# Kernel optimization log

Hardware: AMD Instinct MI355X
Metric: run time of the kernel (lower is better)

## Reference

```python
import jax, jax.numpy as jnp
import numpy as np

NUM_SKILLS = 1000
DIM_S = 64
SIZE_M = 64
B, T = 64, 200


def setup_inputs() -> dict:
    key = jax.random.key(0)
    ks = jax.random.split(key, 16)
    skills = jax.random.randint(ks[0], (B, T), 0, NUM_SKILLS)
    responses = jax.random.randint(ks[1], (B, T), 0, 2)
    s = 1.0 / np.sqrt(DIM_S)
    return {
        "skills": skills,
        "responses": responses,
        "k_emb": jax.random.normal(ks[2], (NUM_SKILLS, DIM_S)) * s,
        "v_emb": jax.random.normal(ks[3], (2 * NUM_SKILLS, DIM_S)) * s,
        "Mk": jax.random.normal(ks[4], (SIZE_M, DIM_S)) * np.sqrt(2.0 / DIM_S),
        "Mv0": jax.random.normal(ks[5], (SIZE_M, DIM_S)) * np.sqrt(2.0 / DIM_S),
        "fW": jax.random.normal(ks[6], (DIM_S, 2 * DIM_S)) * (1.0 / np.sqrt(2 * DIM_S)),
        "fb": jnp.zeros((DIM_S,)),
        "eW": jax.random.normal(ks[7], (DIM_S, DIM_S)) * s,
        "eb": jnp.zeros((DIM_S,)),
        "aW": jax.random.normal(ks[8], (DIM_S, DIM_S)) * s,
        "ab": jnp.zeros((DIM_S,)),
        "pW": jax.random.normal(ks[9], (1, DIM_S)) * s,
        "pb": jnp.zeros((1,)),
    }


def reference(skills, responses, k_emb, v_emb, Mk, Mv0, fW, fb, eW, eb, aW, ab, pW, pb):
    # dropout is identity in eval mode
    masked_r = responses * (responses > -1).astype(responses.dtype)
    x = skills + NUM_SKILLS * masked_r            # [B, T]
    k = k_emb[skills]                              # [B, T, D]
    v = v_emb[x]                                   # [B, T, D]
    w = jax.nn.softmax(jnp.einsum('btd,md->btm', k, Mk), axis=-1)  # [B, T, M]
    e = jax.nn.sigmoid(v @ eW.T + eb)              # [B, T, D]
    a = jnp.tanh(v @ aW.T + ab)                    # [B, T, D]

    Mv_init = jnp.broadcast_to(Mv0, (skills.shape[0],) + Mv0.shape)  # [B, M, D]

    def step(Mvt, inp):
        wt, et, at = inp                           # [B,M], [B,D], [B,D]
        read = jnp.einsum('bm,bmd->bd', wt, Mvt)   # read BEFORE update (Mv[:, :-1])
        Mvt = Mvt * (1.0 - wt[:, :, None] * et[:, None, :]) + wt[:, :, None] * at[:, None, :]
        return Mvt, read

    xs = (jnp.swapaxes(w, 0, 1), jnp.swapaxes(e, 0, 1), jnp.swapaxes(a, 0, 1))
    _, reads = jax.lax.scan(step, Mv_init, xs)     # reads: [T, B, D]
    reads = jnp.swapaxes(reads, 0, 1)              # [B, T, D]

    f = jnp.tanh(jnp.concatenate([reads, k], axis=-1) @ fW.T + fb)  # [B, T, D]
    p = jax.nn.sigmoid(f @ pW.T + pb)[..., 0]      # [B, T]
    return p[:, 1:]                                # pred, [B, T-1]
```

## Files before the change

kernel.cpp:

```cpp
#include <hip/hip_runtime.h>
#include <stdint.h>

#define NSK 1000
#define TT  200
#define BB  64
#define NROW (BB * TT)
#define NOUT (BB * (TT-1))
#define CH  20
#define RW  4

__device__ __forceinline__ unsigned ulane_bcast(unsigned v, int l) {
  return __builtin_amdgcn_readlane(v, l);
}
__device__ __forceinline__ float frcp(float x) { return __builtin_amdgcn_rcpf(x); }
__device__ __forceinline__ float sigm(float x) { return frcp(1.f + __expf(-x)); }
__device__ __forceinline__ float tanh_fast(float x) {
  return fmaf(-2.f, frcp(1.f + __expf(2.f * x)), 1.f);
}

typedef _Float16 half2v __attribute__((ext_vector_type(2)));
typedef _Float16 v8h __attribute__((ext_vector_type(8)));
typedef float    v4f __attribute__((ext_vector_type(4)));
union H2U { unsigned u; half2v h; };
__device__ __forceinline__ unsigned pack2h(float a, float b) {
  H2U x; x.h = (half2v){(_Float16)a, (_Float16)b}; return x.u;
}
__device__ __forceinline__ unsigned short f16bits(float x) {
  H2U u; u.h = (half2v){(_Float16)x, (_Float16)0.f}; return (unsigned short)(u.u & 0xffffu);
}
__device__ __forceinline__ float f16lo(unsigned bits) {
  H2U u; u.u = bits; return (float)u.h.x;
}
__device__ __forceinline__ float f16hi(unsigned bits) {
  H2U u; u.u = bits; return (float)u.h.y;
}
__device__ __forceinline__ float dot2h(unsigned sp, unsigned wp, float acc) {
#if __has_builtin(__builtin_amdgcn_fdot2)
  H2U s, w; s.u = sp; w.u = wp;
  return __builtin_amdgcn_fdot2(s.h, w.h, acc, false);
#else
  H2U s, w; s.u = sp; w.u = wp;
  return fmaf((float)s.h.y, (float)w.h.y, fmaf((float)s.h.x, (float)w.h.x, acc));
#endif
}
__device__ __forceinline__ unsigned pack_pairs(float v) {
  const int lane = threadIdx.x & 63;
  float a = __shfl(v, 2 * lane);
  float b = __shfl(v, 2 * lane + 1);
  return pack2h(a, b);
}
__device__ __forceinline__ v8h pk8(float4 x0, float4 x1) {
  return (v8h){(_Float16)x0.x, (_Float16)x0.y, (_Float16)x0.z, (_Float16)x0.w,
               (_Float16)x1.x, (_Float16)x1.y, (_Float16)x1.z, (_Float16)x1.w};
}

__global__ __launch_bounds__(128) void wea_mfma(
    const int* __restrict__ skills, const int* __restrict__ responses,
    const float* __restrict__ k_emb, const float* __restrict__ v_emb,
    const float* __restrict__ Mk, const float* __restrict__ eW,
    const float* __restrict__ eb, const float* __restrict__ aW,
    const float* __restrict__ ab,
    unsigned* __restrict__ ea_ws, unsigned short* __restrict__ w16_ws)
{
  const int tid  = threadIdx.x;
  const int wv   = tid >> 6, lane = tid & 63;
  const int tile = blockIdx.x * 2 + wv;
  const int r0   = tile * 16;
  const int lr   = lane & 15;
  const int lg   = lane >> 4;

  const int sk = skills[r0 + lr];
  int rr = responses[r0 + lr]; rr = (rr > -1) ? rr : 0;
  const int vrow = sk + NSK * rr;

  const float4* kq = (const float4*)(k_emb + (size_t)sk * 64);
  const float4* vq = (const float4*)(v_emb + (size_t)vrow * 64);
  v8h ak[2], av[2];
  #pragma unroll
  for (int t = 0; t < 2; ++t) {
    const int o = t * 8 + lg * 2;
    ak[t] = pk8(kq[o], kq[o + 1]);
    av[t] = pk8(vq[o], vq[o + 1]);
  }

  float ebv[4], abv[4];
  #pragma unroll
  for (int c = 0; c < 4; ++c) { ebv[c] = eb[16 * c + lr]; abv[c] = ab[16 * c + lr]; }

  v4f acK[4], acE[4], acA[4];
  #pragma unroll
  for (int c = 0; c < 4; ++c) {
    acK[c] = (v4f){0.f, 0.f, 0.f, 0.f};
    acE[c] = (v4f){0.f, 0.f, 0.f, 0.f};
    acA[c] = (v4f){0.f, 0.f, 0.f, 0.f};
  }

  #pragma unroll
  for (int c = 0; c < 4; ++c) {
    const float4* mq = (const float4*)(Mk + (size_t)(16 * c + lr) * 64);
    const float4* eq = (const float4*)(eW + (size_t)(16 * c + lr) * 64);
    const float4* aq = (const float4*)(aW + (size_t)(16 * c + lr) * 64);
    #pragma unroll
    for (int t = 0; t < 2; ++t) {
      const int o = t * 8 + lg * 2;
      const v8h bm = pk8(mq[o], mq[o + 1]);
      const v8h be = pk8(eq[o], eq[o + 1]);
      const v8h ba = pk8(aq[o], aq[o + 1]);
      acK[c] = __builtin_amdgcn_mfma_f32_16x16x32_f16(ak[t], bm, acK[c], 0, 0, 0);
      acE[c] = __builtin_amdgcn_mfma_f32_16x16x32_f16(av[t], be, acE[c], 0, 0, 0);
      acA[c] = __builtin_amdgcn_mfma_f32_16x16x32_f16(av[t], ba, acA[c], 0, 0, 0);
    }
  }

  float rs[4];
  #pragma unroll
  for (int q = 0; q < 4; ++q) {
    float m = fmaxf(fmaxf(acK[0][q], acK[1][q]), fmaxf(acK[2][q], acK[3][q]));
    #pragma unroll
    for (int off = 8; off; off >>= 1) m = fmaxf(m, __shfl_xor(m, off));
    float s = 0.f;
    #pragma unroll
    for (int c = 0; c < 4; ++c) {
      acK[c][q] = __expf(acK[c][q] - m);
      s += acK[c][q];
    }
    #pragma unroll
    for (int off = 8; off; off >>= 1) s += __shfl_xor(s, off);
    rs[q] = frcp(s);
  }

  #pragma unroll
  for (int c = 0; c < 4; ++c) {
    const int j = 16 * c + lr;
    #pragma unroll
    for (int q = 0; q < 4; ++q) {
      const int row = r0 + lg * 4 + q;
      w16_ws[(size_t)row * 64 + j] = f16bits(acK[c][q] * rs[q]);
      const float ev = sigm(acE[c][q] + ebv[c]);
      const float avv = tanh_fast(acA[c][q] + abv[c]);
      ea_ws[(size_t)row * 64 + j] = pack2h(ev, avv);
    }
  }
}

__device__ __forceinline__ void load_chunk(
    const unsigned* __restrict__ eap, const unsigned short* __restrict__ wp,
    int t0, int wl, int lane, unsigned* eab, unsigned* wvb)
{
  #pragma unroll
  for (int k = 0; k < CH; ++k) {
    eab[k] = eap[(t0 + k) * 64 + lane];
    wvb[k] = (unsigned)wp[(t0 + k) * 64 + wl];
  }
}

__device__ __forceinline__ void compute_chunk(
    float* Mv, const unsigned* eab, const unsigned* wvb,
    float* __restrict__ red, int wave, int lane)
{
  #pragma unroll
  for (int k = 0; k < CH; ++k) {
    const float ev = f16lo(eab[k]), av = f16hi(eab[k]);
    float rp = 0.f;
    #pragma unroll
    for (int i = 0; i < RW; ++i) {
      const float wm = f16lo(ulane_bcast(wvb[k], i));
      rp = fmaf(wm, Mv[i], rp);
      float tp = fmaf(-ev, Mv[i], av);
      Mv[i] = fmaf(wm, tp, Mv[i]);
    }
    red[k * 256 + wave * 64 + lane] = rp;
  }
}

__device__ __forceinline__ void reduce_store(
    const float* __restrict__ red, int ch, int base, int wave, int lane,
    unsigned short* __restrict__ ps)
{
  #pragma unroll
  for (int u = 0; u < 5; ++u) {
    const int k = wave * 5 + u;
    const float* rr = red + k * 256;
    const float v = (rr[lane] + rr[64 + lane]) + (rr[128 + lane] + rr[192 + lane]);
    ps[(size_t)(base + ch * CH + k) * 64 + lane] = f16bits(v);
  }
}

__global__ __launch_bounds__(256) void scan_kernel(
    const float* __restrict__ Mv0,
    const unsigned* __restrict__ ea_ws, const unsigned short* __restrict__ w16_ws,
    unsigned short* __restrict__ p0, unsigned short* __restrict__ p1,
    unsigned short* __restrict__ p2, unsigned short* __restrict__ p3)
{
  __shared__ float red[2][CH * 256];
  const int b    = blockIdx.x >> 2;
  const int s    = blockIdx.x & 3;
  const int wave = threadIdx.x >> 6;
  const int lane = threadIdx.x & 63;
  const int base = b * TT;
  const int m0   = s * 16 + wave * RW;
  const int wl   = m0 + (lane & (RW - 1));
  unsigned short* ps = (s == 0) ? p0 : (s == 1) ? p1 : (s == 2) ? p2 : p3;

  float Mv[RW];
  #pragma unroll
  for (int i = 0; i < RW; ++i) Mv[i] = Mv0[(size_t)(m0 + i) * 64 + lane];

  const unsigned* eap = ea_ws + (size_t)base * 64;
  const unsigned short* wp = w16_ws + (size_t)base * 64;

  unsigned ea0[CH], wv0[CH], ea1[CH], wv1[CH];
  load_chunk(eap, wp, 0, wl, lane, ea0, wv0);
  for (int ch = 0; ch < TT / CH; ch += 2) {
    if ((ch + 1) * CH < TT)
      load_chunk(eap, wp, (ch + 1) * CH, wl, lane, ea1, wv1);
    compute_chunk(Mv, ea0, wv0, red[0], wave, lane);
    __syncthreads();
    reduce_store(red[0], ch, base, wave, lane, ps);
    if ((ch + 2) * CH < TT)
      load_chunk(eap, wp, (ch + 2) * CH, wl, lane, ea0, wv0);
    if ((ch + 1) * CH < TT) {
      compute_chunk(Mv, ea1, wv1, red[1], wave, lane);
      __syncthreads();
      reduce_store(red[1], ch + 1, base, wave, lane, ps);
    }
  }
}

__global__ __launch_bounds__(256) void fp_kernel(
    const int* __restrict__ skills, const float* __restrict__ k_emb,
    const float* __restrict__ fW, const float* __restrict__ fb,
    const float* __restrict__ pW, const float* __restrict__ pb,
    const unsigned short* __restrict__ p0, const unsigned short* __restrict__ p1,
    const unsigned short* __restrict__ p2, const unsigned short* __restrict__ p3,
    float* __restrict__ out)
{
  __shared__ unsigned sf[64 * 72];
  const int tid = threadIdx.x;
  for (int ch = tid; ch < 1024; ch += 256) {
    const int j = ch >> 4, cc = ch & 15;
    const float4 f0 = ((const float4*)fW)[j * 32 + cc * 2];
    const float4 f1 = ((const float4*)fW)[j * 32 + cc * 2 + 1];
    uint4 pk;
    pk.x = pack2h(f0.x, f0.y); pk.y = pack2h(f0.z, f0.w);
    pk.z = pack2h(f1.x, f1.y); pk.w = pack2h(f1.z, f1.w);
    *(uint4*)&sf[j * 72 + ((cc + j) & 15) * 4] = pk;
  }
  __syncthreads();

  const int wave = tid >> 6, lane = tid & 63;
  const float fbl = fb[lane], pwl = pW[lane], pb0 = pb[0];
  const int p = blockIdx.x * 4 + wave;

  float rv[2], kc[2];
  int bsave[2], tsave[2];
  #pragma unroll
  for (int i = 0; i < 2; ++i) {
    const unsigned idx = 2u * p + i;
    const unsigned b = idx / 199u;
    const int row = (int)(idx + b + 1u);
    bsave[i] = (int)b; tsave[i] = (int)(idx - b * 199u);
    rv[i] = (f16lo((unsigned)p0[(size_t)row * 64 + lane])
           + f16lo((unsigned)p1[(size_t)row * 64 + lane]))
          + (f16lo((unsigned)p2[(size_t)row * 64 + lane])
           + f16lo((unsigned)p3[(size_t)row * 64 + lane]));
    kc[i] = k_emb[(size_t)skills[row] * 64 + lane];
  }
  unsigned rvp[2], kvp[2];
  #pragma unroll
  for (int i = 0; i < 2; ++i) {
    rvp[i] = pack_pairs(rv[i]);
    kvp[i] = pack_pairs(kc[i]);
  }

  float acc[2] = {fbl, fbl};
  #pragma unroll 1
  for (int h = 0; h < 4; ++h) {
    uint4 qf[4];
    #pragma unroll
    for (int c = 0; c < 4; ++c)
      qf[c] = *(const uint4*)&sf[lane * 72 + (((h * 4 + c) + lane) & 15) * 4];
    #pragma unroll
    for (int i = 0; i < 2; ++i) {
      #pragma unroll
      for (int c = 0; c < 4; ++c) {
        const unsigned uu[4] = {qf[c].x, qf[c].y, qf[c].z, qf[c].w};
        #pragma unroll
        for (int m = 0; m < 4; ++m) {
          const int idx = (h * 4 + c) * 4 + m;
          const unsigned sp = (idx < 32) ? ulane_bcast(rvp[i], idx)
                                         : ulane_bcast(kvp[i], idx - 32);
          acc[i] = dot2h(sp, uu[m], acc[i]);
        }
      }
    }
  }

  float f0 = tanh_fast(acc[0]) * pwl;
  float f1 = tanh_fast(acc[1]) * pwl;
  #pragma unroll
  for (int off = 32; off; off >>= 1) {
    f0 += __shfl_xor(f0, off);
    f1 += __shfl_xor(f1, off);
  }
  if (lane == 0) {
    out[(size_t)bsave[0] * (TT - 1) + tsave[0]] = sigm(f0 + pb0);
    out[(size_t)bsave[1] * (TT - 1) + tsave[1]] = sigm(f1 + pb0);
  }
}

extern "C" void kernel_launch(void* const* d_in, const int* in_sizes, int n_in,
                              void* d_out, int out_size, void* d_ws, size_t ws_size,
                              hipStream_t stream) {
  const int* skills    = (const int*)d_in[0];
  const int* responses = (const int*)d_in[1];
  const float* k_emb   = (const float*)d_in[2];
  const float* v_emb   = (const float*)d_in[3];
  const float* Mk      = (const float*)d_in[4];
  const float* Mv0     = (const float*)d_in[5];
  const float* fW      = (const float*)d_in[6];
  const float* fb      = (const float*)d_in[7];
  const float* eW      = (const float*)d_in[8];
  const float* eb      = (const float*)d_in[9];
  const float* aW      = (const float*)d_in[10];
  const float* ab      = (const float*)d_in[11];
  const float* pW      = (const float*)d_in[12];
  const float* pb      = (const float*)d_in[13];

  unsigned* ea_ws        = (unsigned*)d_ws;
  unsigned short* w16_ws = (unsigned short*)(ea_ws + (size_t)NROW * 64);
  unsigned short* p0     = w16_ws + (size_t)NROW * 64;
  unsigned short* p1     = p0 + (size_t)NROW * 64;
  unsigned short* p2     = p1 + (size_t)NROW * 64;
  unsigned short* p3     = p2 + (size_t)NROW * 64;

  wea_mfma<<<dim3(400), 128, 0, stream>>>(
      skills, responses, k_emb, v_emb, Mk, eW, eb, aW, ab, ea_ws, w16_ws);
  scan_kernel<<<dim3(BB * 4), 256, 0, stream>>>(Mv0, ea_ws, w16_ws, p0, p1, p2, p3);
  fp_kernel<<<dim3(NOUT / 8), 256, 0, stream>>>(
      skills, k_emb, fW, fb, pW, pb, p0, p1, p2, p3, (float*)d_out);
}
```

Before: 121.9 us.

## Split scan over eight memory slices and move final projection to MFMA

The scan kernel now splits the 64 memory rows across 8 blocks per batch instead of 4, with 2 rows per wave, which doubles the number of blocks working on the sequential recurrence. The final f/p projection is rewritten as a 16x16x32 f16 MFMA GEMM that sums the eight partial read slices in fp16, replacing the per-lane dot2 readlane loop. The cost is more partial-sum traffic (8 slices) and fp16 accumulation of the partials, which may add some precision loss.

```diff
diff --git a/kernel.cpp b/kernel.cpp
--- a/kernel.cpp
+++ b/kernel.cpp
@@ -7,7 +7,9 @@
 #define NROW (BB * TT)
 #define NOUT (BB * (TT-1))
 #define CH  20
-#define RW  4
+#define RW  2
+#define NSPLIT 8
+#define PSTR ((size_t)NROW * 64)
 
 __device__ __forceinline__ unsigned ulane_bcast(unsigned v, int l) {
   return __builtin_amdgcn_readlane(v, l);
@@ -22,6 +24,7 @@
 typedef _Float16 v8h __attribute__((ext_vector_type(8)));
 typedef float    v4f __attribute__((ext_vector_type(4)));
 union H2U { unsigned u; half2v h; };
+union V8U { uint4 u; v8h h; };
 __device__ __forceinline__ unsigned pack2h(float a, float b) {
   H2U x; x.h = (half2v){(_Float16)a, (_Float16)b}; return x.u;
 }
@@ -33,21 +36,6 @@
 }
 __device__ __forceinline__ float f16hi(unsigned bits) {
   H2U u; u.u = bits; return (float)u.h.y;
-}
-__device__ __forceinline__ float dot2h(unsigned sp, unsigned wp, float acc) {
-#if __has_builtin(__builtin_amdgcn_fdot2)
-  H2U s, w; s.u = sp; w.u = wp;
-  return __builtin_amdgcn_fdot2(s.h, w.h, acc, false);
-#else
-  H2U s, w; s.u = sp; w.u = wp;
-  return fmaf((float)s.h.y, (float)w.h.y, fmaf((float)s.h.x, (float)w.h.x, acc));
-#endif
-}
-__device__ __forceinline__ unsigned pack_pairs(float v) {
-  const int lane = threadIdx.x & 63;
-  float a = __shfl(v, 2 * lane);
-  float b = __shfl(v, 2 * lane + 1);
-  return pack2h(a, b);
 }
 __device__ __forceinline__ v8h pk8(float4 x0, float4 x1) {
   return (v8h){(_Float16)x0.x, (_Float16)x0.y, (_Float16)x0.z, (_Float16)x0.w,
@@ -189,18 +177,17 @@
 __global__ __launch_bounds__(256) void scan_kernel(
     const float* __restrict__ Mv0,
     const unsigned* __restrict__ ea_ws, const unsigned short* __restrict__ w16_ws,
-    unsigned short* __restrict__ p0, unsigned short* __restrict__ p1,
-    unsigned short* __restrict__ p2, unsigned short* __restrict__ p3)
+    unsigned short* __restrict__ pbase)
 {
   __shared__ float red[2][CH * 256];
-  const int b    = blockIdx.x >> 2;
-  const int s    = blockIdx.x & 3;
+  const int b    = blockIdx.x >> 3;
+  const int s    = blockIdx.x & 7;
   const int wave = threadIdx.x >> 6;
   const int lane = threadIdx.x & 63;
   const int base = b * TT;
-  const int m0   = s * 16 + wave * RW;
+  const int m0   = s * 8 + wave * RW;
   const int wl   = m0 + (lane & (RW - 1));
-  unsigned short* ps = (s == 0) ? p0 : (s == 1) ? p1 : (s == 2) ? p2 : p3;
+  unsigned short* ps = pbase + (size_t)s * PSTR;
 
   float Mv[RW];
   #pragma unroll
@@ -227,85 +214,80 @@
   }
 }
 
-__global__ __launch_bounds__(256) void fp_kernel(
+__global__ __launch_bounds__(256) void fp_mfma(
     const int* __restrict__ skills, const float* __restrict__ k_emb,
     const float* __restrict__ fW, const float* __restrict__ fb,
     const float* __restrict__ pW, const float* __restrict__ pb,
-    const unsigned short* __restrict__ p0, const unsigned short* __restrict__ p1,
-    const unsigned short* __restrict__ p2, const unsigned short* __restrict__ p3,
+    const unsigned short* __restrict__ pbase,
     float* __restrict__ out)
 {
-  __shared__ unsigned sf[64 * 72];
-  const int tid = threadIdx.x;
-  for (int ch = tid; ch < 1024; ch += 256) {
-    const int j = ch >> 4, cc = ch & 15;
-    const float4 f0 = ((const float4*)fW)[j * 32 + cc * 2];
-    const float4 f1 = ((const float4*)fW)[j * 32 + cc * 2 + 1];
-    uint4 pk;
-    pk.x = pack2h(f0.x, f0.y); pk.y = pack2h(f0.z, f0.w);
-    pk.z = pack2h(f1.x, f1.y); pk.w = pack2h(f1.z, f1.w);
-    *(uint4*)&sf[j * 72 + ((cc + j) & 15) * 4] = pk;
-  }
-  __syncthreads();
-
-  const int wave = tid >> 6, lane = tid & 63;
-  const float fbl = fb[lane], pwl = pW[lane], pb0 = pb[0];
-  const int p = blockIdx.x * 4 + wave;
-
-  float rv[2], kc[2];
-  int bsave[2], tsave[2];
-  #pragma unroll
-  for (int i = 0; i < 2; ++i) {
-    const unsigned idx = 2u * p + i;
-    const unsigned b = idx / 199u;
-    const int row = (int)(idx + b + 1u);
-    bsave[i] = (int)b; tsave[i] = (int)(idx - b * 199u);
-    rv[i] = (f16lo((unsigned)p0[(size_t)row * 64 + lane])
-           + f16lo((unsigned)p1[(size_t)row * 64 + lane]))
-          + (f16lo((unsigned)p2[(size_t)row * 64 + lane])
-           + f16lo((unsigned)p3[(size_t)row * 64 + lane]));
-    kc[i] = k_emb[(size_t)skills[row] * 64 + lane];
-  }
-  unsigned rvp[2], kvp[2];
-  #pragma unroll
-  for (int i = 0; i < 2; ++i) {
-    rvp[i] = pack_pairs(rv[i]);
-    kvp[i] = pack_pairs(kc[i]);
-  }
-
-  float acc[2] = {fbl, fbl};
-  #pragma unroll 1
-  for (int h = 0; h < 4; ++h) {
-    uint4 qf[4];
+  const int tid  = threadIdx.x;
+  const int wv   = tid >> 6, lane = tid & 63;
+  const int lr   = lane & 15;
+  const int lg   = lane >> 4;
+  const int o0   = (blockIdx.x * 4 + wv) * 16;
+
+  const unsigned idx = o0 + lr;
+  const unsigned bb  = idx / 199u;
+  const unsigned t2  = idx - bb * 199u;
+  const int srow     = (int)(idx + bb + 1u);
+
+  v8h ar[4];
+  #pragma unroll
+  for (int t = 0; t < 2; ++t) {
+    const size_t eo = (size_t)srow * 64 + t * 32 + lg * 8;
+    V8U s0, s1, s2, s3;
+    s0.u = *(const uint4*)&pbase[eo];
+    s1.u = *(const uint4*)&pbase[eo + PSTR];
+    s2.u = *(const uint4*)&pbase[eo + 2 * PSTR];
+    s3.u = *(const uint4*)&pbase[eo + 3 * PSTR];
+    v8h acc = (s0.h + s1.h) + (s2.h + s3.h);
+    s0.u = *(const uint4*)&pbase[eo + 4 * PSTR];
+    s1.u = *(const uint4*)&pbase[eo + 5 * PSTR];
+    s2.u = *(const uint4*)&pbase[eo + 6 * PSTR];
+    s3.u = *(const uint4*)&pbase[eo + 7 * PSTR];
+    ar[t] = acc + ((s0.h + s1.h) + (s2.h + s3.h));
+  }
+  {
+    const float4* kq = (const float4*)(k_emb + (size_t)skills[srow] * 64);
+    #pragma unroll
+    for (int t = 2; t < 4; ++t) {
+      const int o = (t - 2) * 8 + lg * 2;
+      ar[t] = pk8(kq[o], kq[o + 1]);
+    }
+  }
+
+  float fbv[4], pwv[4];
+  #pragma unroll
+  for (int c = 0; c < 4; ++c) { fbv[c] = fb[16 * c + lr]; pwv[c] = pW[16 * c + lr]; }
+
+  v4f acc[4];
+  #pragma unroll
+  for (int c = 0; c < 4; ++c) acc[c] = (v4f){0.f, 0.f, 0.f, 0.f};
+
+  const float4* fq = (const float4*)fW;
+  #pragma unroll
+  for (int c = 0; c < 4; ++c) {
+    const int jb = (16 * c + lr) * 32;
+    #pragma unroll
+    for (int t = 0; t < 4; ++t) {
+      const int o = jb + t * 8 + lg * 2;
+      const v8h bf = pk8(fq[o], fq[o + 1]);
+      acc[c] = __builtin_amdgcn_mfma_f32_16x16x32_f16(ar[t], bf, acc[c], 0, 0, 0);
+    }
+  }
+
+  const float pb0 = pb[0];
+  #pragma unroll
+  for (int q = 0; q < 4; ++q) {
+    float s = 0.f;
     #pragma unroll
     for (int c = 0; c < 4; ++c)
-      qf[c] = *(const uint4*)&sf[lane * 72 + (((h * 4 + c) + lane) & 15) * 4];
-    #pragma unroll
-    for (int i = 0; i < 2; ++i) {
-      #pragma unroll
-      for (int c = 0; c < 4; ++c) {
-        const unsigned uu[4] = {qf[c].x, qf[c].y, qf[c].z, qf[c].w};
-        #pragma unroll
-        for (int m = 0; m < 4; ++m) {
-          const int idx = (h * 4 + c) * 4 + m;
-          const unsigned sp = (idx < 32) ? ulane_bcast(rvp[i], idx)
-                                         : ulane_bcast(kvp[i], idx - 32);
-          acc[i] = dot2h(sp, uu[m], acc[i]);
-        }
-      }
-    }
-  }
-
-  float f0 = tanh_fast(acc[0]) * pwl;
-  float f1 = tanh_fast(acc[1]) * pwl;
-  #pragma unroll
-  for (int off = 32; off; off >>= 1) {
-    f0 += __shfl_xor(f0, off);
-    f1 += __shfl_xor(f1, off);
-  }
-  if (lane == 0) {
-    out[(size_t)bsave[0] * (TT - 1) + tsave[0]] = sigm(f0 + pb0);
-    out[(size_t)bsave[1] * (TT - 1) + tsave[1]] = sigm(f1 + pb0);
+      s += tanh_fast(acc[c][q] + fbv[c]) * pwv[c];
+    #pragma unroll
+    for (int off = 8; off; off >>= 1) s += __shfl_xor(s, off);
+    if (lr == lg * 4 + q)
+      out[(size_t)bb * (TT - 1) + t2] = sigm(s + pb0);
   }
 }
 
@@ -326,17 +308,15 @@
   const float* ab      = (const float*)d_in[11];
   const float* pW      = (const float*)d_in[12];
   const float* pb      = (const float*)d_in[13];
+  (void)in_sizes; (void)n_in; (void)out_size; (void)ws_size;
 
   unsigned* ea_ws        = (unsigned*)d_ws;
   unsigned short* w16_ws = (unsigned short*)(ea_ws + (size_t)NROW * 64);
-  unsigned short* p0     = w16_ws + (size_t)NROW * 64;
-  unsigned short* p1     = p0 + (size_t)NROW * 64;
-  unsigned short* p2     = p1 + (size_t)NROW * 64;
-  unsigned short* p3     = p2 + (size_t)NROW * 64;
+  unsigned short* pbase  = w16_ws + PSTR;
 
   wea_mfma<<<dim3(400), 128, 0, stream>>>(
       skills, responses, k_emb, v_emb, Mk, eW, eb, aW, ab, ea_ws, w16_ws);
-  scan_kernel<<<dim3(BB * 4), 256, 0, stream>>>(Mv0, ea_ws, w16_ws, p0, p1, p2, p3);
-  fp_kernel<<<dim3(NOUT / 8), 256, 0, stream>>>(
-      skills, k_emb, fW, fb, pW, pb, p0, p1, p2, p3, (float*)d_out);
-}
+  scan_kernel<<<dim3(BB * NSPLIT), 256, 0, stream>>>(Mv0, ea_ws, w16_ws, pbase);
+  fp_mfma<<<dim3(199), 256, 0, stream>>>(
+      skills, k_emb, fW, fb, pW, pb, pbase, (float*)d_out);
+}
```

New measurement: 119.9 us. Within noise of the previous version (-1.7%).
